# Optimization experiments

Measured on AMD Instinct MI355X. Metric: run time of the kernel, lower is better.

Reference implementation:

```python
import jax, jax.numpy as jnp
import numpy as np

BETA = 0.25  # commitment_beta


def setup_inputs() -> dict:
    key = jax.random.key(0)
    k1, k2 = jax.random.split(key)
    B, S, D, K = 4, 2048, 256, 8192
    z_e = jax.random.normal(k1, (B, S, D), dtype=jnp.float32)
    # codebook init ~ uniform(-1/K, 1/K) in the original; scale is irrelevant for correctness,
    # use normal scaled similarly small.
    codebook = jax.random.uniform(k2, (K, D), dtype=jnp.float32, minval=-1.0 / K, maxval=1.0 / K)
    return {"z_e": z_e, "codebook": codebook}


def reference(z_e, codebook):
    B, S, D = z_e.shape
    flat = z_e.reshape(-1, D)  # [N, D], N = B*S
    distances = (
        jnp.sum(flat * flat, axis=1, keepdims=True)
        - 2.0 * (flat @ codebook.T)
        + jnp.sum(codebook * codebook, axis=1)[None, :]
    )
    indices = jnp.argmin(distances, axis=1)  # [N]
    z_q = codebook[indices].reshape(B, S, D)
    codebook_loss = jnp.mean((jax.lax.stop_gradient(z_e) - z_q) ** 2)
    commitment_loss = jnp.mean((z_e - jax.lax.stop_gradient(z_q)) ** 2)
    vq_loss = codebook_loss + BETA * commitment_loss
    # straight-through estimator
    z_q_st = z_e + jax.lax.stop_gradient(z_q - z_e)
    return z_q_st, indices.reshape(B, S), vq_loss
```

## Files before the change

kernel.cpp:

```cpp
#include <hip/hip_runtime.h>
#include <stdint.h>

#define N_ROWS  8192
#define DIM     256
#define K_CODES 8192
#define SPLITK  8
#define KS      1024
#define NT      128
#define LSLOTS  16
#define GSLOTS  12
#define MARGIN_ACC 1.0e-4f

typedef unsigned long long u64;
typedef unsigned short u16;
typedef short s16x8 __attribute__((ext_vector_type(8)));
typedef float f32x4 __attribute__((ext_vector_type(4)));

__device__ __forceinline__ u64 u64min(u64 a, u64 b) { return a < b ? a : b; }

__device__ __forceinline__ u16 f2bf(float f) {
    unsigned u = __float_as_uint(f);
    u += 0x7fffu + ((u >> 16) & 1u);
    return (u16)(u >> 16);
}

__device__ __forceinline__ void gld16(void* lds, const void* g) {
    __builtin_amdgcn_global_load_lds(
        (const __attribute__((address_space(1))) unsigned int*)g,
        (__attribute__((address_space(3))) unsigned int*)lds, 16, 0, 0);
}

__global__ __launch_bounds__(256) void vq_prep(const float* __restrict__ z_e,
                                               const float* __restrict__ cb,
                                               u16* __restrict__ zb,
                                               u16* __restrict__ cbb,
                                               float* __restrict__ xnorm,
                                               float* __restrict__ cnorm) {
    int wid  = (blockIdx.x * 256 + threadIdx.x) >> 6;
    int lane = threadIdx.x & 63;
    const float* src; u16* d16; float* dn;
    if (wid < N_ROWS) { src = z_e + (size_t)wid * DIM; d16 = zb + (size_t)wid * DIM; dn = xnorm + wid; }
    else              { int k = wid - N_ROWS;
                        src = cb  + (size_t)k   * DIM; d16 = cbb + (size_t)k * DIM; dn = cnorm + k; }
    float4 v = *(const float4*)(src + lane * 4);
    ushort4 h;
    h.x = f2bf(v.x); h.y = f2bf(v.y); h.z = f2bf(v.z); h.w = f2bf(v.w);
    *(ushort4*)(d16 + lane * 4) = h;
    float s = (v.x * v.x + v.y * v.y) + (v.z * v.z + v.w * v.w);
#pragma unroll
    for (int off = 1; off < 64; off <<= 1)
        s += __shfl_xor(s, off, 64);
    if (lane == 0) *dn = s;
}

__global__ __launch_bounds__(256) void vq_mfma(const u16* __restrict__ zb,
                                               const u16* __restrict__ cbb,
                                               int* __restrict__ cand_cnt,
                                               int* __restrict__ cand_idx) {
    __shared__ u16   Xs[128 * 64];
    __shared__ u16   Cs[128 * 64];
    __shared__ float lcd[128 * LSLOTS];
    __shared__ int   lci[128 * LSLOTS];
    __shared__ int   lcnt[128];
    __shared__ float gmaxs[2][128];

    const int tid   = threadIdx.x;
    const int lane  = tid & 63;
    const int wave  = tid >> 6;
    const int wm    = wave & 1;
    const int wn    = wave >> 1;
    const int quad  = lane >> 4;
    const int l16   = lane & 15;
    const int split = blockIdx.x;
    const int n0    = blockIdx.y * 128;

    if (tid < 128) lcnt[tid] = 0;

    const int srow8  = lane >> 3;
    const int schunk = lane & 7;
    const int ssw    = (schunk ^ srow8) * 8;

    float runmax[16];
#pragma unroll
    for (int t = 0; t < 16; t++) runmax[t] = -3.0e38f;

    for (int kt = 0; kt < KS / NT; kt++) {
        const int kbase = split * KS + kt * NT;
        f32x4 acc[4][4];
#pragma unroll
        for (int i = 0; i < 4; i++)
#pragma unroll
            for (int j = 0; j < 4; j++)
#pragma unroll
                for (int e = 0; e < 4; e++) acc[i][j][e] = 0.0f;

        for (int kc = 0; kc < 4; kc++) {
            __syncthreads();
#pragma unroll
            for (int t = 0; t < 4; t++) {
                int rg = wave * 4 + t;
                int r  = rg * 8 + srow8;
                gld16(&Xs[rg * 512], zb  + (size_t)(n0 + r)    * DIM + kc * 64 + ssw);
                gld16(&Cs[rg * 512], cbb + (size_t)(kbase + r) * DIM + kc * 64 + ssw);
            }
            __syncthreads();
#pragma unroll
            for (int ks = 0; ks < 2; ks++) {
                s16x8 af[4], bfr[4];
#pragma unroll
                for (int i = 0; i < 4; i++)
                    af[i] = *(const s16x8*)&Xs[(wm * 64 + i * 16 + l16) * 64 +
                                               (((ks << 2) | quad) ^ (l16 & 7)) * 8];
#pragma unroll
                for (int j = 0; j < 4; j++)
                    bfr[j] = *(const s16x8*)&Cs[(wn * 64 + j * 16 + l16) * 64 +
                                                (((ks << 2) | quad) ^ (l16 & 7)) * 8];
#pragma unroll
                for (int i = 0; i < 4; i++)
#pragma unroll
                    for (int j = 0; j < 4; j++)
                        acc[i][j] = __builtin_amdgcn_mfma_f32_16x16x32_bf16(af[i], bfr[j], acc[i][j], 0, 0, 0);
            }
        }

#pragma unroll
        for (int i = 0; i < 4; i++)
#pragma unroll
            for (int r = 0; r < 4; r++) {
                float m = fmaxf(fmaxf(acc[i][0][r], acc[i][1][r]),
                                fmaxf(acc[i][2][r], acc[i][3][r]));
                m = fmaxf(m, __shfl_xor(m, 1, 64));
                m = fmaxf(m, __shfl_xor(m, 2, 64));
                m = fmaxf(m, __shfl_xor(m, 4, 64));
                m = fmaxf(m, __shfl_xor(m, 8, 64));
                runmax[i * 4 + r] = fmaxf(runmax[i * 4 + r], m);
                float thr = runmax[i * 4 + r] - MARGIN_ACC;
                int rl = wm * 64 + i * 16 + quad * 4 + r;
#pragma unroll
                for (int j = 0; j < 4; j++) {
                    float d = acc[i][j][r];
                    if (d >= thr) {
                        int pos = atomicAdd(&lcnt[rl], 1);
                        if (pos < LSLOTS) {
                            lcd[rl * LSLOTS + pos] = d;
                            lci[rl * LSLOTS + pos] = kbase + wn * 64 + j * 16 + l16;
                        }
                    }
                }
            }
    }

    if (l16 == 0) {
#pragma unroll
        for (int i = 0; i < 4; i++)
#pragma unroll
            for (int r = 0; r < 4; r++)
                gmaxs[wn][wm * 64 + i * 16 + quad * 4 + r] = runmax[i * 4 + r];
    }
    __syncthreads();

    if (tid < 128) {
        int n   = n0 + tid;
        int cnt = lcnt[tid]; if (cnt > LSLOTS) cnt = LSLOTS;
        float thrf = fmaxf(gmaxs[0][tid], gmaxs[1][tid]) - MARGIN_ACC;
        int base = (n * SPLITK + split) * GSLOTS;
        int w = 0;
        for (int s = 0; s < cnt && w < GSLOTS; s++)
            if (lcd[tid * LSLOTS + s] >= thrf)
                cand_idx[base + w++] = lci[tid * LSLOTS + s];
        cand_cnt[n * SPLITK + split] = w;
    }
}

__global__ __launch_bounds__(256) void vq_finalize(const float* __restrict__ z_e,
                                                   const float* __restrict__ cb,
                                                   const float* __restrict__ xnorm,
                                                   const float* __restrict__ cnorm,
                                                   const int* __restrict__ cand_cnt,
                                                   const int* __restrict__ cand_idx,
                                                   float* __restrict__ out_zq,
                                                   float* __restrict__ out_idx,
                                                   float* __restrict__ rowloss) {
    const int n    = blockIdx.x * 4 + (threadIdx.x >> 6);
    const int lane = threadIdx.x & 63;

    int myidx = -1;
    int t = 0;
#pragma unroll
    for (int s = 0; s < SPLITK; s++) {
        int c = cand_cnt[n * SPLITK + s];
        if (lane >= t && lane < t + c)
            myidx = cand_idx[(n * SPLITK + s) * GSLOTS + (lane - t)];
        t += c;
    }

    u64 key = ~0ULL;
    if (myidx >= 0) {
        const float* xr = z_e + (size_t)n * DIM;
        const float* cr = cb + (size_t)myidx * DIM;
        float acc = 0.0f;
#pragma unroll 8
        for (int d = 0; d < DIM; d++)
            acc = __builtin_fmaf(xr[d], cr[d], acc);
        float dist = __builtin_fmaf(-2.0f, acc, xnorm[n]) + cnorm[myidx];
        key = ((u64)__float_as_uint(dist) << 32) | (unsigned)myidx;
    }
#pragma unroll
    for (int off = 1; off < 64; off <<= 1)
        key = u64min(key, __shfl_xor(key, off, 64));

    int idx = (int)(unsigned)(key & 0xffffffffu);
    if (key == ~0ULL) idx = 0;

    float4 x = *(const float4*)(z_e + (size_t)n * DIM + lane * 4);
    float4 c = *(const float4*)(cb + (size_t)idx * DIM + lane * 4);
    float4 st;
    st.x = x.x + (c.x - x.x); st.y = x.y + (c.y - x.y);
    st.z = x.z + (c.z - x.z); st.w = x.w + (c.w - x.w);
    *(float4*)(out_zq + (size_t)n * DIM + lane * 4) = st;

    float d0 = x.x - c.x, d1 = x.y - c.y, d2 = x.z - c.z, d3 = x.w - c.w;
    float s2 = (d0 * d0 + d1 * d1) + (d2 * d2 + d3 * d3);
#pragma unroll
    for (int off = 1; off < 64; off <<= 1)
        s2 += __shfl_xor(s2, off, 64);
    if (lane == 0) {
        rowloss[n] = s2;
        out_idx[n] = (float)idx;
    }
}

__global__ __launch_bounds__(256) void vq_loss(const float* __restrict__ rowloss,
                                               float* __restrict__ out_loss) {
    __shared__ double sd[256];
    double s = 0.0;
    for (int i = threadIdx.x; i < N_ROWS; i += 256) s += (double)rowloss[i];
    sd[threadIdx.x] = s;
    __syncthreads();
    for (int off = 128; off; off >>= 1) {
        if (threadIdx.x < off) sd[threadIdx.x] += sd[threadIdx.x + off];
        __syncthreads();
    }
    if (threadIdx.x == 0) {
        double mean = sd[0] / (double)((size_t)N_ROWS * DIM);
        out_loss[0] = (float)(1.25 * mean);
    }
}

extern "C" void kernel_launch(void* const* d_in, const int* in_sizes, int n_in,
                              void* d_out, int out_size, void* d_ws, size_t ws_size,
                              hipStream_t stream) {
    const float* z_e = (const float*)d_in[0];
    const float* cb  = (const float*)d_in[1];

    float* out   = (float*)d_out;
    float* zq    = out;
    float* oidx  = out + (size_t)N_ROWS * DIM;
    float* oloss = oidx + N_ROWS;

    u16*   zb       = (u16*)d_ws;
    u16*   cbb      = zb + (size_t)N_ROWS * DIM;
    float* xnorm    = (float*)(cbb + (size_t)K_CODES * DIM);
    float* cnorm    = xnorm + N_ROWS;
    float* rowloss  = cnorm + K_CODES;
    int*   cand_cnt = (int*)(rowloss + N_ROWS);
    int*   cand_idx = cand_cnt + N_ROWS * SPLITK;

    vq_prep    <<<(N_ROWS + K_CODES) / 4, 256, 0, stream>>>(z_e, cb, zb, cbb, xnorm, cnorm);
    vq_mfma    <<<dim3(SPLITK, N_ROWS / 128), 256, 0, stream>>>(zb, cbb, cand_cnt, cand_idx);
    vq_finalize<<<N_ROWS / 4, 256, 0, stream>>>(z_e, cb, xnorm, cnorm, cand_cnt, cand_idx, zq, oidx, rowloss);
    vq_loss    <<<1, 256, 0, stream>>>(rowloss, oloss);
}
```

Measured before the change: 196.6 us.

## Keep X fragments in registers and triple-buffer codebook tiles in LDS

The X tile is now loaded once into registers (32 bf16 fragments per lane) instead of being restaged into LDS for every K tile. The codebook tile uses a three-deep LDS ring buffer with async global-to-LDS loads issued two stages ahead, and each stage ends with a single vmcnt wait plus barrier instead of two __syncthreads. This targets load latency stalls and redundant X traffic, at the cost of much higher VGPR pressure, now capped by launch_bounds(256,2), which risks spills.

```diff
diff --git a/kernel.cpp b/kernel.cpp
--- a/kernel.cpp
+++ b/kernel.cpp
@@ -53,12 +53,11 @@
     if (lane == 0) *dn = s;
 }
 
-__global__ __launch_bounds__(256) void vq_mfma(const u16* __restrict__ zb,
-                                               const u16* __restrict__ cbb,
-                                               int* __restrict__ cand_cnt,
-                                               int* __restrict__ cand_idx) {
-    __shared__ u16   Xs[128 * 64];
-    __shared__ u16   Cs[128 * 64];
+__global__ __launch_bounds__(256, 2) void vq_mfma(const u16* __restrict__ zb,
+                                                  const u16* __restrict__ cbb,
+                                                  int* __restrict__ cand_cnt,
+                                                  int* __restrict__ cand_idx) {
+    __shared__ u16   Cs[3][128 * 64];
     __shared__ float lcd[128 * LSLOTS];
     __shared__ int   lci[128 * LSLOTS];
     __shared__ int   lcnt[128];
@@ -79,12 +78,38 @@
     const int srow8  = lane >> 3;
     const int schunk = lane & 7;
     const int ssw    = (schunk ^ srow8) * 8;
+    const u16* csrc  = cbb + (size_t)split * KS * DIM + (size_t)srow8 * DIM + ssw;
+
+    s16x8 af[4][8];
+#pragma unroll
+    for (int i = 0; i < 4; i++) {
+        const u16* p = zb + (size_t)(n0 + wm * 64 + i * 16 + l16) * DIM + quad * 8;
+#pragma unroll
+        for (int s = 0; s < 8; s++)
+            af[i][s] = *(const s16x8*)(p + s * 32);
+    }
+
+    auto STAGE = [&](int s, int bw) {
+        const u16* src = csrc + (size_t)(s >> 2) * (NT * DIM) + (s & 3) * 64;
+#pragma unroll
+        for (int t = 0; t < 4; t++) {
+            int rg = wave * 4 + t;
+            gld16(&Cs[bw][rg * 512], src + (size_t)rg * (8 * DIM));
+        }
+    };
 
     float runmax[16];
 #pragma unroll
     for (int t = 0; t < 16; t++) runmax[t] = -3.0e38f;
 
-    for (int kt = 0; kt < KS / NT; kt++) {
+    STAGE(0, 0);
+    STAGE(1, 1);
+    asm volatile("s_waitcnt vmcnt(4)" ::: "memory");
+    __builtin_amdgcn_s_barrier();
+
+    int bufR = 0, bufW = 2;
+
+    for (int kt = 0; kt < 8; kt++) {
         const int kbase = split * KS + kt * NT;
         f32x4 acc[4][4];
 #pragma unroll
@@ -94,33 +119,36 @@
 #pragma unroll
                 for (int e = 0; e < 4; e++) acc[i][j][e] = 0.0f;
 
+#pragma unroll
         for (int kc = 0; kc < 4; kc++) {
-            __syncthreads();
-#pragma unroll
-            for (int t = 0; t < 4; t++) {
-                int rg = wave * 4 + t;
-                int r  = rg * 8 + srow8;
-                gld16(&Xs[rg * 512], zb  + (size_t)(n0 + r)    * DIM + kc * 64 + ssw);
-                gld16(&Cs[rg * 512], cbb + (size_t)(kbase + r) * DIM + kc * 64 + ssw);
+            const int it = (kt << 2) | kc;
+            if (it < 30) STAGE(it + 2, bufW);
+
+            const u16* cbuf = &Cs[bufR][0];
+#pragma unroll
+            for (int ks = 0; ks < 2; ks++) {
+                s16x8 bfr[4];
+#pragma unroll
+                for (int j = 0; j < 4; j++)
+                    bfr[j] = *(const s16x8*)&cbuf[(wn * 64 + j * 16 + l16) * 64 +
+                                                  (((ks << 2) | quad) ^ (l16 & 7)) * 8];
+#pragma unroll
+                for (int i = 0; i < 4; i++)
+#pragma unroll
+                    for (int j = 0; j < 4; j++)
+                        acc[i][j] = __builtin_amdgcn_mfma_f32_16x16x32_bf16(
+                            af[i][kc * 2 + ks], bfr[j], acc[i][j], 0, 0, 0);
             }
-            __syncthreads();
-#pragma unroll
-            for (int ks = 0; ks < 2; ks++) {
-                s16x8 af[4], bfr[4];
-#pragma unroll
-                for (int i = 0; i < 4; i++)
-                    af[i] = *(const s16x8*)&Xs[(wm * 64 + i * 16 + l16) * 64 +
-                                               (((ks << 2) | quad) ^ (l16 & 7)) * 8];
-#pragma unroll
-                for (int j = 0; j < 4; j++)
-                    bfr[j] = *(const s16x8*)&Cs[(wn * 64 + j * 16 + l16) * 64 +
-                                                (((ks << 2) | quad) ^ (l16 & 7)) * 8];
-#pragma unroll
-                for (int i = 0; i < 4; i++)
-#pragma unroll
-                    for (int j = 0; j < 4; j++)
-                        acc[i][j] = __builtin_amdgcn_mfma_f32_16x16x32_bf16(af[i], bfr[j], acc[i][j], 0, 0, 0);
+
+            if (it < 30) {
+                asm volatile("s_waitcnt vmcnt(4)" ::: "memory");
+                __builtin_amdgcn_s_barrier();
+            } else if (it == 30) {
+                asm volatile("s_waitcnt vmcnt(0)" ::: "memory");
+                __builtin_amdgcn_s_barrier();
             }
+            bufR = bufR == 2 ? 0 : bufR + 1;
+            bufW = bufW == 2 ? 0 : bufW + 1;
         }
 
 #pragma unroll
```

New measurement: 197.7 us. About the same (+0.6%).

## Keep query rows in registers and stream codebook directly from global memory

Applied to the files above, without the earlier changes.

Replaces the LDS-staged tiled GEMM with a scheme where each wave loads its 32 query rows once into registers, for the whole row dimension, and reads codebook fragments straight from global memory into MFMA operands. The LDS staging and its per-chunk barriers disappear. Split-K doubles to 16 with smaller code slices, and the candidate buffers move to a split-major layout. The aim is to cut barrier and LDS overhead and raise occupancy, at the cost of uncoalesced global codebook reads that depend on L1/L2 reuse, and fewer candidate slots per split.

```diff
diff --git a/kernel.cpp b/kernel.cpp
--- a/kernel.cpp
+++ b/kernel.cpp
@@ -4,11 +4,11 @@
 #define N_ROWS  8192
 #define DIM     256
 #define K_CODES 8192
-#define SPLITK  8
-#define KS      1024
+#define SPLITK  16
+#define KS      512
 #define NT      128
 #define LSLOTS  16
-#define GSLOTS  12
+#define GSLOTS  8
 #define MARGIN_ACC 1.0e-4f
 
 typedef unsigned long long u64;
@@ -22,12 +22,6 @@
     unsigned u = __float_as_uint(f);
     u += 0x7fffu + ((u >> 16) & 1u);
     return (u16)(u >> 16);
-}
-
-__device__ __forceinline__ void gld16(void* lds, const void* g) {
-    __builtin_amdgcn_global_load_lds(
-        (const __attribute__((address_space(1))) unsigned int*)g,
-        (__attribute__((address_space(3))) unsigned int*)lds, 16, 0, 0);
 }
 
 __global__ __launch_bounds__(256) void vq_prep(const float* __restrict__ z_e,
@@ -53,22 +47,18 @@
     if (lane == 0) *dn = s;
 }
 
-__global__ __launch_bounds__(256) void vq_mfma(const u16* __restrict__ zb,
-                                               const u16* __restrict__ cbb,
-                                               int* __restrict__ cand_cnt,
-                                               int* __restrict__ cand_idx) {
-    __shared__ u16   Xs[128 * 64];
-    __shared__ u16   Cs[128 * 64];
+__global__ __launch_bounds__(256, 3) void vq_mfma(const u16* __restrict__ zb,
+                                                  const u16* __restrict__ cbb,
+                                                  int* __restrict__ cand_cnt,
+                                                  int* __restrict__ cand_idx) {
     __shared__ float lcd[128 * LSLOTS];
     __shared__ int   lci[128 * LSLOTS];
     __shared__ int   lcnt[128];
-    __shared__ float gmaxs[2][128];
+    __shared__ float gmaxs[128];
 
     const int tid   = threadIdx.x;
     const int lane  = tid & 63;
     const int wave  = tid >> 6;
-    const int wm    = wave & 1;
-    const int wn    = wave >> 1;
     const int quad  = lane >> 4;
     const int l16   = lane & 15;
     const int split = blockIdx.x;
@@ -76,99 +66,101 @@
 
     if (tid < 128) lcnt[tid] = 0;
 
-    const int srow8  = lane >> 3;
-    const int schunk = lane & 7;
-    const int ssw    = (schunk ^ srow8) * 8;
-
-    float runmax[16];
-#pragma unroll
-    for (int t = 0; t < 16; t++) runmax[t] = -3.0e38f;
+    s16x8 af[2][8];
+#pragma unroll
+    for (int i = 0; i < 2; i++) {
+        const u16* p = zb + (size_t)(n0 + wave * 32 + i * 16 + l16) * DIM + quad * 8;
+#pragma unroll
+        for (int s = 0; s < 8; s++)
+            af[i][s] = *(const s16x8*)(p + s * 32);
+    }
+
+    __syncthreads();
+
+    float runmax[8];
+#pragma unroll
+    for (int t = 0; t < 8; t++) runmax[t] = -3.0e38f;
 
     for (int kt = 0; kt < KS / NT; kt++) {
         const int kbase = split * KS + kt * NT;
-        f32x4 acc[4][4];
-#pragma unroll
-        for (int i = 0; i < 4; i++)
-#pragma unroll
-            for (int j = 0; j < 4; j++)
-#pragma unroll
-                for (int e = 0; e < 4; e++) acc[i][j][e] = 0.0f;
-
-        for (int kc = 0; kc < 4; kc++) {
-            __syncthreads();
-#pragma unroll
-            for (int t = 0; t < 4; t++) {
-                int rg = wave * 4 + t;
-                int r  = rg * 8 + srow8;
-                gld16(&Xs[rg * 512], zb  + (size_t)(n0 + r)    * DIM + kc * 64 + ssw);
-                gld16(&Cs[rg * 512], cbb + (size_t)(kbase + r) * DIM + kc * 64 + ssw);
+#pragma unroll
+        for (int jg = 0; jg < 2; jg++) {
+            const int cb0 = kbase + jg * 64;
+            const u16* rp0 = cbb + (size_t)(cb0 + l16) * DIM + quad * 8;
+            const u16* rp1 = rp0 + 16 * DIM;
+            const u16* rp2 = rp0 + 32 * DIM;
+            const u16* rp3 = rp0 + 48 * DIM;
+
+            f32x4 acc[2][4];
+#pragma unroll
+            for (int i = 0; i < 2; i++)
+#pragma unroll
+                for (int j = 0; j < 4; j++)
+#pragma unroll
+                    for (int e = 0; e < 4; e++) acc[i][j][e] = 0.0f;
+
+#pragma unroll
+            for (int s = 0; s < 8; s++) {
+                s16x8 b0 = *(const s16x8*)(rp0 + s * 32);
+                s16x8 b1 = *(const s16x8*)(rp1 + s * 32);
+                s16x8 b2 = *(const s16x8*)(rp2 + s * 32);
+                s16x8 b3 = *(const s16x8*)(rp3 + s * 32);
+#pragma unroll
+                for (int i = 0; i < 2; i++) {
+                    acc[i][0] = __builtin_amdgcn_mfma_f32_16x16x32_bf16(af[i][s], b0, acc[i][0], 0, 0, 0);
+                    acc[i][1] = __builtin_amdgcn_mfma_f32_16x16x32_bf16(af[i][s], b1, acc[i][1], 0, 0, 0);
+                    acc[i][2] = __builtin_amdgcn_mfma_f32_16x16x32_bf16(af[i][s], b2, acc[i][2], 0, 0, 0);
+                    acc[i][3] = __builtin_amdgcn_mfma_f32_16x16x32_bf16(af[i][s], b3, acc[i][3], 0, 0, 0);
+                }
             }
-            __syncthreads();
-#pragma unroll
-            for (int ks = 0; ks < 2; ks++) {
-                s16x8 af[4], bfr[4];
-#pragma unroll
-                for (int i = 0; i < 4; i++)
-                    af[i] = *(const s16x8*)&Xs[(wm * 64 + i * 16 + l16) * 64 +
-                                               (((ks << 2) | quad) ^ (l16 & 7)) * 8];
-#pragma unroll
-                for (int j = 0; j < 4; j++)
-                    bfr[j] = *(const s16x8*)&Cs[(wn * 64 + j * 16 + l16) * 64 +
-                                                (((ks << 2) | quad) ^ (l16 & 7)) * 8];
-#pragma unroll
-                for (int i = 0; i < 4; i++)
-#pragma unroll
-                    for (int j = 0; j < 4; j++)
-                        acc[i][j] = __builtin_amdgcn_mfma_f32_16x16x32_bf16(af[i], bfr[j], acc[i][j], 0, 0, 0);
-            }
-        }
-
-#pragma unroll
-        for (int i = 0; i < 4; i++)
-#pragma unroll
-            for (int r = 0; r < 4; r++) {
-                float m = fmaxf(fmaxf(acc[i][0][r], acc[i][1][r]),
-                                fmaxf(acc[i][2][r], acc[i][3][r]));
-                m = fmaxf(m, __shfl_xor(m, 1, 64));
-                m = fmaxf(m, __shfl_xor(m, 2, 64));
-                m = fmaxf(m, __shfl_xor(m, 4, 64));
-                m = fmaxf(m, __shfl_xor(m, 8, 64));
-                runmax[i * 4 + r] = fmaxf(runmax[i * 4 + r], m);
-                float thr = runmax[i * 4 + r] - MARGIN_ACC;
-                int rl = wm * 64 + i * 16 + quad * 4 + r;
-#pragma unroll
-                for (int j = 0; j < 4; j++) {
-                    float d = acc[i][j][r];
-                    if (d >= thr) {
-                        int pos = atomicAdd(&lcnt[rl], 1);
-                        if (pos < LSLOTS) {
-                            lcd[rl * LSLOTS + pos] = d;
-                            lci[rl * LSLOTS + pos] = kbase + wn * 64 + j * 16 + l16;
+
+#pragma unroll
+            for (int i = 0; i < 2; i++)
+#pragma unroll
+                for (int r = 0; r < 4; r++) {
+                    float m = fmaxf(fmaxf(acc[i][0][r], acc[i][1][r]),
+                                    fmaxf(acc[i][2][r], acc[i][3][r]));
+                    m = fmaxf(m, __shfl_xor(m, 1, 64));
+                    m = fmaxf(m, __shfl_xor(m, 2, 64));
+                    m = fmaxf(m, __shfl_xor(m, 4, 64));
+                    m = fmaxf(m, __shfl_xor(m, 8, 64));
+                    runmax[i * 4 + r] = fmaxf(runmax[i * 4 + r], m);
+                    float thr = runmax[i * 4 + r] - MARGIN_ACC;
+                    int rl = wave * 32 + i * 16 + quad * 4 + r;
+#pragma unroll
+                    for (int j = 0; j < 4; j++) {
+                        float d = acc[i][j][r];
+                        if (d >= thr) {
+                            int pos = atomicAdd(&lcnt[rl], 1);
+                            if (pos < LSLOTS) {
+                                lcd[rl * LSLOTS + pos] = d;
+                                lci[rl * LSLOTS + pos] = cb0 + j * 16 + l16;
+                            }
                         }
                     }
                 }
-            }
+        }
     }
 
     if (l16 == 0) {
 #pragma unroll
-        for (int i = 0; i < 4; i++)
+        for (int i = 0; i < 2; i++)
 #pragma unroll
             for (int r = 0; r < 4; r++)
-                gmaxs[wn][wm * 64 + i * 16 + quad * 4 + r] = runmax[i * 4 + r];
+                gmaxs[wave * 32 + i * 16 + quad * 4 + r] = runmax[i * 4 + r];
     }
     __syncthreads();
 
     if (tid < 128) {
         int n   = n0 + tid;
         int cnt = lcnt[tid]; if (cnt > LSLOTS) cnt = LSLOTS;
-        float thrf = fmaxf(gmaxs[0][tid], gmaxs[1][tid]) - MARGIN_ACC;
-        int base = (n * SPLITK + split) * GSLOTS;
+        float thrf = gmaxs[tid] - MARGIN_ACC;
+        int base = (split * N_ROWS + n) * GSLOTS;
         int w = 0;
         for (int s = 0; s < cnt && w < GSLOTS; s++)
             if (lcd[tid * LSLOTS + s] >= thrf)
                 cand_idx[base + w++] = lci[tid * LSLOTS + s];
-        cand_cnt[n * SPLITK + split] = w;
+        cand_cnt[split * N_ROWS + n] = w;
     }
 }
 
@@ -188,9 +180,9 @@
     int t = 0;
 #pragma unroll
     for (int s = 0; s < SPLITK; s++) {
-        int c = cand_cnt[n * SPLITK + s];
+        int c = cand_cnt[s * N_ROWS + n];
         if (lane >= t && lane < t + c)
-            myidx = cand_idx[(n * SPLITK + s) * GSLOTS + (lane - t)];
+            myidx = cand_idx[(s * N_ROWS + n) * GSLOTS + (lane - t)];
         t += c;
     }
 
```

New measurement: 273.7 us. 1.39x slower.
